# Kernel tuning notes

Hardware: AMD Instinct MI355X
Metric: run time of the kernel (lower is better)

## Reference

```python
import jax, jax.numpy as jnp
import numpy as np
from jax import lax


def ternarize(w):
    # TWN-style ternarization: threshold delta = 0.7*mean|w|, scale alpha =
    # mean |w| over surviving entries; straight-through in backward.
    aw = jnp.abs(w)
    delta = 0.7 * jnp.mean(aw)
    mask = (aw > delta).astype(w.dtype)
    alpha = jnp.sum(aw * mask) / jnp.maximum(jnp.sum(mask), 1.0)
    q = alpha * jnp.sign(w) * mask
    return w + lax.stop_gradient(q - w)


def conv2d(x, w, b):
    # x: [N,C,H,W], w: [O,I,kh,kw]
    y = lax.conv_general_dilated(x, w, window_strides=(1, 1), padding='VALID',
                                 dimension_numbers=('NCHW', 'OIHW', 'NCHW'))
    return y + b[None, :, None, None]


def maxpool2(x):
    return lax.reduce_window(x, -jnp.inf, lax.max,
                             window_dimensions=(1, 1, 2, 2),
                             window_strides=(1, 1, 2, 2), padding='VALID')


def setup_inputs() -> dict:
    key = jax.random.key(0)
    ks = jax.random.split(key, 11)
    n_classes = 10
    x = jax.random.normal(ks[0], (1024, 1, 32, 32), dtype=jnp.float32)
    # Kaiming-ish scaled params
    w1 = jax.random.normal(ks[1], (32, 1, 5, 5), jnp.float32) * (1.0 / np.sqrt(1 * 25))
    b1 = jnp.zeros((32,), jnp.float32)
    w2 = jax.random.normal(ks[2], (64, 32, 5, 5), jnp.float32) * (1.0 / np.sqrt(32 * 25))
    b2 = jnp.zeros((64,), jnp.float32)
    w3 = jax.random.normal(ks[3], (120, 64, 5, 5), jnp.float32) * (1.0 / np.sqrt(64 * 25))
    b3 = jnp.zeros((120,), jnp.float32)
    fw1 = jax.random.normal(ks[4], (84, 120), jnp.float32) * (1.0 / np.sqrt(120))
    fb1 = jnp.zeros((84,), jnp.float32)
    fw2 = jax.random.normal(ks[5], (n_classes, 84), jnp.float32) * (1.0 / np.sqrt(84))
    fb2 = jnp.zeros((n_classes,), jnp.float32)
    return {"x": x, "w1": w1, "b1": b1, "w2": w2, "b2": b2,
            "w3": w3, "b3": b3, "fw1": fw1, "fb1": fb1, "fw2": fw2, "fb2": fb2}


def reference(x, w1, b1, w2, b2, w3, b3, fw1, fb1, fw2, fb2):
    h = jnp.tanh(conv2d(x, ternarize(w1), b1))   # [N,32,28,28]
    h = maxpool2(h)                              # [N,32,14,14]
    h = jnp.tanh(conv2d(h, ternarize(w2), b2))   # [N,64,10,10]
    h = maxpool2(h)                              # [N,64,5,5]
    h = jnp.tanh(conv2d(h, ternarize(w3), b3))   # [N,120,1,1]
    h = h.reshape(h.shape[0], -1)                # [N,120]
    h = jnp.tanh(h @ ternarize(fw1).T + fb1)     # [N,84]
    logits = h @ ternarize(fw2).T + fb2          # [N,n_classes]
    probs = jax.nn.softmax(logits, axis=1)
    return (logits, probs)
```

## Files before the change

kernel.cpp:

```cpp
#include <hip/hip_runtime.h>
#include <hip/hip_bf16.h>
#include <math.h>


typedef __attribute__((ext_vector_type(8))) short bf16x8;
typedef __attribute__((ext_vector_type(4))) float f32x4;

static const size_t OFF_PB    = 0;
static const size_t OFF_W1B   = 256;
static const size_t OFF_W2B   = 1056;
static const size_t OFF_W3B   = 26656;
static const size_t OFF_FW1T  = 129056;
static const size_t OFF_FW2T  = 139136;
static const size_t OFF_P2B   = 139976;
static const size_t OFF_H3    = 959176;

#define BPT 16

__device__ __forceinline__ ushort f2bf(float v) {
    unsigned u = __float_as_uint(v);
    unsigned r = (u + 0x7FFFu + ((u >> 16) & 1u)) >> 16;
    return (ushort)r;
}
__device__ __forceinline__ float bf2f(ushort h) {
    return __uint_as_float((unsigned)h << 16);
}

__device__ __forceinline__ float tanh_fast(float x) {
    float e = __expf(-2.0f * fabsf(x));
    float r = 1.0f - 2.0f * e / (1.0f + e);
    return copysignf(r, x);
}

__device__ __forceinline__ void tensor_select(int tensor,
        const float* w1, const float* w2, const float* w3,
        const float* fw1, const float* fw2,
        const float*& src, int& O, int& K) {
    switch (tensor) {
        case 0: src = w1;  O = 32;  K = 25;   break;
        case 1: src = w2;  O = 64;  K = 800;  break;
        case 2: src = w3;  O = 120; K = 1600; break;
        case 3: src = fw1; O = 84;  K = 120;  break;
        default: src = fw2; O = 10; K = 84;   break;
    }
}

__device__ __forceinline__ float block_sum_256(float v, float* sbuf) {
    #pragma unroll
    for (int off = 32; off > 0; off >>= 1) v += __shfl_down(v, off);
    const int wid = threadIdx.x >> 6;
    if ((threadIdx.x & 63) == 0) sbuf[wid] = v;
    __syncthreads();
    return sbuf[0] + sbuf[1] + sbuf[2] + sbuf[3];
}

__device__ __forceinline__ float alpha_of(const float* pb, int tensor) {
    float s1 = 0.f, c = 0.f;
    #pragma unroll
    for (int i = 0; i < BPT; ++i) {
        s1 += pb[80 + tensor * BPT + i];
        c  += pb[160 + tensor * BPT + i];
    }
    return s1 / fmaxf(c, 1.0f);
}

__global__ __launch_bounds__(256)
void tern_pass1(const float* w1, const float* w2, const float* w3,
                const float* fw1, const float* fw2, float* pb) {
    __shared__ float sbuf[4];
    const int tensor = blockIdx.x / BPT;
    const int blk    = blockIdx.x % BPT;
    const float* src; int O, K;
    tensor_select(tensor, w1, w2, w3, fw1, fw2, src, O, K);
    const int n = O * K;
    float s = 0.f;
    for (int i = blk * 256 + threadIdx.x; i < n; i += BPT * 256)
        s += fabsf(src[i]);
    s = block_sum_256(s, sbuf);
    if (threadIdx.x == 0) pb[tensor * BPT + blk] = s;
}

__global__ __launch_bounds__(256)
void tern_pass2(const float* w1, const float* w2, const float* w3,
                const float* fw1, const float* fw2,
                ushort* w1b, ushort* w2b, ushort* w3b,
                float* fw1t, float* fw2t, float* pb) {
    __shared__ float sbuf[4];
    const int tensor = blockIdx.x / BPT;
    const int blk    = blockIdx.x % BPT;
    const float* src; int O, K;
    tensor_select(tensor, w1, w2, w3, fw1, fw2, src, O, K);
    const int n = O * K;
    float tot = 0.f;
    #pragma unroll
    for (int i = 0; i < BPT; ++i) tot += pb[tensor * BPT + i];
    const float delta = 0.7f * tot / (float)n;

    const ushort BP = 0x3F80u, BN = 0xBF80u;
    float s1 = 0.f, cnt = 0.f;

    if (tensor == 0) {
        for (int j = blk * 256 + threadIdx.x; j < 1024; j += BPT * 256) {
            const int oc = j >> 5, kk = j & 31;
            ushort qb = 0;
            if (kk < 25) {
                float w = src[oc * 25 + kk];
                float aw = fabsf(w);
                if (aw > delta) { s1 += aw; cnt += 1.f; qb = (w > 0.f) ? BP : BN; }
            }
            w1b[j] = qb;
        }
    } else if (tensor == 2) {
        for (int i = blk * 256 + threadIdx.x; i < 128 * 1600; i += BPT * 256) {
            ushort qb = 0;
            if (i < n) {
                float w = src[i];
                float aw = fabsf(w);
                if (aw > delta) { s1 += aw; cnt += 1.f; qb = (w > 0.f) ? BP : BN; }
            }
            w3b[i] = qb;
        }
    } else if (tensor == 1) {
        for (int i = blk * 256 + threadIdx.x; i < n; i += BPT * 256) {
            float w = src[i];
            float aw = fabsf(w);
            ushort qb = 0;
            if (aw > delta) { s1 += aw; cnt += 1.f; qb = (w > 0.f) ? BP : BN; }
            int oc = i / 800;
            int r  = i - oc * 800;
            int ic = r / 25;
            int tap = r - ic * 25;
            w2b[oc * 800 + tap * 32 + ic] = qb;
        }
    } else {
        float* dst = (tensor == 3) ? fw1t : fw2t;
        for (int i = blk * 256 + threadIdx.x; i < n; i += BPT * 256) {
            float w = src[i];
            float aw = fabsf(w);
            float q = 0.f;
            if (aw > delta) { s1 += aw; cnt += 1.f; q = (w > 0.f) ? 1.f : -1.f; }
            int o = i / K;
            int k = i - o * K;
            dst[k * O + o] = q;
        }
    }
    s1 = block_sum_256(s1, sbuf);
    __syncthreads();
    cnt = block_sum_256(cnt, sbuf);
    if (threadIdx.x == 0) {
        pb[80 + tensor * BPT + blk]  = s1;
        pb[160 + tensor * BPT + blk] = cnt;
    }
}

#define C2PF 4
__device__ __forceinline__ void conv2_all(
        const ushort* __restrict__ w2b, const ushort* sxt,
        int n0, int mt0, int lane, f32x4 acc[4][2]) {
    const int col = lane & 15, quad = lane >> 4;
    const ushort* abase[4];
    #pragma unroll
    for (int mi = 0; mi < 4; ++mi) {
        int m = (mt0 + mi) * 16 + col;
        m = m < 100 ? m : 99;
        const int oh = m / 10, ow = m - oh * 10;
        abase[mi] = sxt + (oh * 14 + ow) * 40 + quad * 8;
    }
    const ushort* wb0 = w2b + (size_t)(n0 + col) * 800 + quad * 8;
    const ushort* wb1 = wb0 + 16 * 800;
    bf16x8 pb0[C2PF], pb1[C2PF];
    #pragma unroll
    for (int i = 0; i < C2PF; ++i) {
        pb0[i] = *(const bf16x8*)(wb0 + i * 32);
        pb1[i] = *(const bf16x8*)(wb1 + i * 32);
    }
    #pragma unroll
    for (int tap = 0; tap < 25; ++tap) {
        const int slot = tap & (C2PF - 1);
        const bf16x8 b0 = pb0[slot];
        const bf16x8 b1 = pb1[slot];
        if (tap + C2PF < 25) {
            pb0[slot] = *(const bf16x8*)(wb0 + (tap + C2PF) * 32);
            pb1[slot] = *(const bf16x8*)(wb1 + (tap + C2PF) * 32);
        }
        const int kh = tap / 5, kw = tap - kh * 5;
        const int aoff = (kh * 14 + kw) * 40;
        #pragma unroll
        for (int mi = 0; mi < 4; ++mi) {
            bf16x8 af = *(const bf16x8*)(abase[mi] + aoff);
            acc[mi][0] = __builtin_amdgcn_mfma_f32_16x16x32_bf16(af, b0, acc[mi][0], 0, 0, 0);
            acc[mi][1] = __builtin_amdgcn_mfma_f32_16x16x32_bf16(af, b1, acc[mi][1], 0, 0, 0);
        }
    }
}

__global__ __launch_bounds__(256, 4)
void conv12_kernel(const float* __restrict__ x, const ushort* __restrict__ w1b,
                   const float* __restrict__ b1, const ushort* __restrict__ w2b,
                   const float* __restrict__ b2, const float* __restrict__ pb,
                   ushort* __restrict__ p2b) {
    __shared__ __align__(16) char smem[37328];
    ushort* A      = (ushort*)smem;
    float*  hb2    = (float*) smem;
    ushort* sxt    = (ushort*)(smem + 19584);
    ushort* sxb    = (ushort*)(smem + 35264);
    float*  salpha = (float*) (smem + 37312);

    const int n = blockIdx.x;
    const int t = threadIdx.x;
    const int wave = t >> 6, lane = t & 63;
    const int col = lane & 15, quad = lane >> 4;

    bf16x8 B0 = *(const bf16x8*)(w1b + col * 32 + quad * 8);
    bf16x8 B1 = *(const bf16x8*)(w1b + (col + 16) * 32 + quad * 8);
    const float b1a = b1[col];
    const float b1b = b1[col + 16];

    {
        float4 v = ((const float4*)(x + (size_t)n * 1024))[t];
        ushort4 q;
        q.x = f2bf(v.x); q.y = f2bf(v.y); q.z = f2bf(v.z); q.w = f2bf(v.w);
        *(ushort4*)(sxb + t * 4) = q;
        if (t == 0) salpha[0] = alpha_of(pb, 0);
        if (t == 1) salpha[1] = alpha_of(pb, 1);
    }
    __syncthreads();

    const float a1 = salpha[0];
    for (int c = 0; c < 3; ++c) {
        const int tbase = (c == 0) ? 0 : (17 + 16 * (c - 1));
        const int ct    = (c == 0) ? 17 : 16;
        const int pbase = tbase * 16;
        const int rows  = ct * 16;

        for (int r = t; r < rows; r += 256) {
            const int p   = pbase + r;
            const int pb4 = p >> 2, sub = p & 3;
            const int oh = 2 * (pb4 / 14) + (sub >> 1);
            const int ow = 2 * (pb4 % 14) + (sub & 1);
            ushort v[25];
            #pragma unroll
            for (int kh = 0; kh < 5; ++kh) {
                const ushort* rr = sxb + (oh + kh) * 32 + ow;
                v[kh*5+0]=rr[0]; v[kh*5+1]=rr[1]; v[kh*5+2]=rr[2];
                v[kh*5+3]=rr[3]; v[kh*5+4]=rr[4];
            }
            uint2* arow = (uint2*)(A + r * 36);
            #pragma unroll
            for (int j = 0; j < 6; ++j) {
                uint2 w;
                w.x = (unsigned)v[4*j]   | ((unsigned)v[4*j+1] << 16);
                w.y = (unsigned)v[4*j+2] | ((unsigned)v[4*j+3] << 16);
                arow[j] = w;
            }
            uint2 w6; w6.x = (unsigned)v[24]; w6.y = 0u;
            arow[6] = w6;
            uint2 w7; w7.x = 0u; w7.y = 0u;
            arow[7] = w7;
        }
        __syncthreads();

        for (int tl = wave; tl < ct; tl += 4) {
            const ushort* ap = A + (tl * 16 + col) * 36 + quad * 8;
            ushort4 lo = *(const ushort4*)ap;
            ushort4 hi = *(const ushort4*)(ap + 4);
            bf16x8 af;
            af[0]=(short)lo.x; af[1]=(short)lo.y; af[2]=(short)lo.z; af[3]=(short)lo.w;
            af[4]=(short)hi.x; af[5]=(short)hi.y; af[6]=(short)hi.z; af[7]=(short)hi.w;
            f32x4 z = {};
            f32x4 c0 = __builtin_amdgcn_mfma_f32_16x16x32_bf16(af, B0, z, 0, 0, 0);
            f32x4 c1 = __builtin_amdgcn_mfma_f32_16x16x32_bf16(af, B1, z, 0, 0, 0);
            const int pos2 = (pbase >> 2) + tl * 4 + quad;
            const float h01 = bf2f(f2bf(fmaxf(c0[0], c0[1])));
            const float h23 = bf2f(f2bf(fmaxf(c0[2], c0[3])));
            sxt[pos2 * 40 + col] =
                f2bf(tanh_fast(fmaf(a1, fmaxf(h01, h23), b1a)));
            const float g01 = bf2f(f2bf(fmaxf(c1[0], c1[1])));
            const float g23 = bf2f(f2bf(fmaxf(c1[2], c1[3])));
            sxt[pos2 * 40 + col + 16] =
                f2bf(tanh_fast(fmaf(a1, fmaxf(g01, g23), b1b)));
        }
        __syncthreads();
    }

    const int n0  = (wave & 1) * 32;
    const int mt0 = (wave >> 1) * 4;
    f32x4 acc2[4][2] = {};
    conv2_all(w2b, sxt, n0, mt0, lane, acc2);

    {
        #pragma unroll
        for (int mi = 0; mi < 4; ++mi) {
            const int mrow = (mt0 + mi) * 16 + quad * 4;
            if (mrow < 100) {
                #pragma unroll
                for (int np = 0; np < 2; ++np) {
                    const int oc = n0 + np * 16 + col;
                    float2 hm;
                    hm.x = fmaxf(acc2[mi][np][0], acc2[mi][np][1]);
                    hm.y = fmaxf(acc2[mi][np][2], acc2[mi][np][3]);
                    *(float2*)(&hb2[oc * 50 + (mrow >> 1)]) = hm;
                }
            }
        }
    }
    __syncthreads();

    const float a2 = salpha[1];
    for (int idx = t; idx < 1600; idx += 256) {
        const int oc = idx / 25, r = idx - oc * 25;
        const int ph = r / 5, pw = r - ph * 5;
        const float* hb = &hb2[oc * 50 + ph * 10 + pw];
        float m = fmaxf(hb[0], hb[5]);
        p2b[(size_t)n * 1600 + idx] = f2bf(tanh_fast(fmaf(a2, m, b2[oc])));
    }
}

template<int STEPS>
__device__ __forceinline__ void conv3_chunk(const ushort* Abase, const ushort* B0,
                                            f32x4& acc0) {
    #pragma unroll
    for (int s = 0; s < STEPS; ++s) {
        bf16x8 af = *(const bf16x8*)(Abase + s * 32);
        bf16x8 b0 = *(const bf16x8*)(B0 + s * 32);
        acc0 = __builtin_amdgcn_mfma_f32_16x16x32_bf16(af, b0, acc0, 0, 0, 0);
    }
}

__global__ __launch_bounds__(256)
void conv3_mfma(const ushort* __restrict__ p2b, const ushort* __restrict__ w3b,
                const float* __restrict__ b3, const float* __restrict__ pb,
                float* __restrict__ h3) {
    __shared__ float red[4][64][4];
    __shared__ float salpha;
    const int t = threadIdx.x;
    const int wave = t >> 6, lane = t & 63;
    const int mt   = blockIdx.x >> 3;
    const int noct = blockIdx.x & 7;
    const int col = lane & 15, quad = lane >> 4;
    const int kstart = (wave < 2) ? wave * 13 : 26 + (wave - 2) * 12;

    if (t == 0) salpha = alpha_of(pb, 2);

    const ushort* Abase = p2b + (size_t)(mt * 16 + col) * 1600 + kstart * 32 + quad * 8;
    const ushort* B0 = w3b + (size_t)(noct * 16 + col) * 1600 + kstart * 32 + quad * 8;

    f32x4 acc0 = {};
    if (wave < 2) conv3_chunk<13>(Abase, B0, acc0);
    else          conv3_chunk<12>(Abase, B0, acc0);

    #pragma unroll
    for (int r = 0; r < 4; ++r) red[wave][lane][r] = acc0[r];
    __syncthreads();

    {
        const float a3 = salpha;
        const int l = t & 63, vh = t >> 6;
        const int lcol = l & 15, lquad = l >> 4;
        const int img = mt * 16 + lquad * 4 + vh;
        float s = red[0][l][vh] + red[1][l][vh] + red[2][l][vh] + red[3][l][vh];
        const int oc = noct * 16 + lcol;
        if (oc < 120) h3[(size_t)img * 120 + oc] = tanh_fast(fmaf(a3, s, b3[oc]));
    }
}

__global__ __launch_bounds__(128)
void fc_kernel(const float* __restrict__ h3, const float* __restrict__ fw1t,
               const float* __restrict__ fb1, const float* __restrict__ fw2t,
               const float* __restrict__ fb2, const float* __restrict__ pb,
               float* __restrict__ out) {
    const int n = blockIdx.x;
    __shared__ float sh[120];
    __shared__ float sh4[84];
    __shared__ float sl[10];
    __shared__ float salpha[2];
    __shared__ __align__(16) float wbuf[2][30 * 84];
    __shared__ __align__(16) float fw2s[84 * 10];
    const int t = threadIdx.x;
    if (t < 120) sh[t] = h3[(size_t)n * 120 + t];
    if (t == 120) salpha[0] = alpha_of(pb, 3);
    if (t == 121) salpha[1] = alpha_of(pb, 4);
    #pragma unroll
    for (int i = 0; i < 2; ++i) {
        const int j = t + i * 128;
        if (j < 210) ((float4*)fw2s)[j] = ((const float4*)fw2t)[j];
    }
    for (int i = t; i < 630; i += 128)
        ((float4*)wbuf[0])[i] = ((const float4*)fw1t)[i];
    __syncthreads();

    float a = 0.f;
    #pragma unroll
    for (int c = 0; c < 4; ++c) {
        if (c < 3) {
            const float4* src = (const float4*)(fw1t + (c + 1) * 2520);
            float4* dst = (float4*)wbuf[(c + 1) & 1];
            for (int i = t; i < 630; i += 128) dst[i] = src[i];
        }
        if (t < 84) {
            const float* wc = wbuf[c & 1];
            #pragma unroll 6
            for (int kk = 0; kk < 30; ++kk)
                a = fmaf(wc[kk * 84 + t], sh[30 * c + kk], a);
        }
        __syncthreads();
    }
    if (t < 84) sh4[t] = tanh_fast(fmaf(salpha[0], a, fb1[t]));
    __syncthreads();
    if (t < 10) {
        const float af2 = salpha[1];
        float a2 = 0.f;
        #pragma unroll 4
        for (int k = 0; k < 84; ++k) a2 = fmaf(fw2s[k * 10 + t], sh4[k], a2);
        const float lg = fmaf(af2, a2, fb2[t]);
        sl[t] = lg;
        out[(size_t)n * 10 + t] = lg;
    }
    __syncthreads();
    if (t < 10) {
        float m = -INFINITY;
        #pragma unroll
        for (int i = 0; i < 10; ++i) m = fmaxf(m, sl[i]);
        float s = 0.f;
        #pragma unroll
        for (int i = 0; i < 10; ++i) s += expf(sl[i] - m);
        out[10240 + (size_t)n * 10 + t] = expf(sl[t] - m) / s;
    }
}

extern "C" void kernel_launch(void* const* d_in, const int* in_sizes, int n_in,
                              void* d_out, int out_size, void* d_ws, size_t ws_size,
                              hipStream_t stream) {
    const float* x   = (const float*)d_in[0];
    const float* w1  = (const float*)d_in[1];
    const float* b1  = (const float*)d_in[2];
    const float* w2  = (const float*)d_in[3];
    const float* b2  = (const float*)d_in[4];
    const float* w3  = (const float*)d_in[5];
    const float* b3  = (const float*)d_in[6];
    const float* fw1 = (const float*)d_in[7];
    const float* fb1 = (const float*)d_in[8];
    const float* fw2 = (const float*)d_in[9];
    const float* fb2 = (const float*)d_in[10];

    float* ws = (float*)d_ws;
    float*  pb   = ws + OFF_PB;
    ushort* w1b  = (ushort*)(ws + OFF_W1B);
    ushort* w2b  = (ushort*)(ws + OFF_W2B);
    ushort* w3b  = (ushort*)(ws + OFF_W3B);
    float*  fw1t = ws + OFF_FW1T;
    float*  fw2t = ws + OFF_FW2T;
    ushort* p2b  = (ushort*)(ws + OFF_P2B);
    float*  h3   = ws + OFF_H3;
    float*  out  = (float*)d_out;

    tern_pass1<<<5 * BPT, 256, 0, stream>>>(w1, w2, w3, fw1, fw2, pb);
    tern_pass2<<<5 * BPT, 256, 0, stream>>>(w1, w2, w3, fw1, fw2,
                                            w1b, w2b, w3b, fw1t, fw2t, pb);
    conv12_kernel<<<1024, 256, 0, stream>>>(x, w1b, b1, w2b, b2, pb, p2b);
    conv3_mfma<<<512, 256, 0, stream>>>(p2b, w3b, b3, pb, h3);
    fc_kernel<<<1024, 128, 0, stream>>>(h3, fw1t, fb1, fw2t, fb2, pb, out);
}
```

Baseline: 148.9 us.

## Fuse conv3 with FC layers and softmax into one kernel per 16 images

Merges the conv3 MFMA kernel and the per-image FC/softmax kernel into one kernel. Each block handles 16 images and all 8 output-channel tiles, keeps h3 in shared memory, and runs both FC layers and the softmax for those 16 images. This removes the h3 round trip through global memory and one launch, and it loads the FC weights once per 16 images instead of once per image. In exchange the grid shrinks from 512 and 1024 blocks to 64 blocks, which leaves most CUs idle, and the scalar FC loops are serialized within each block.

```diff
diff --git a/kernel.cpp b/kernel.cpp
--- a/kernel.cpp
+++ b/kernel.cpp
@@ -13,7 +13,6 @@
 static const size_t OFF_FW1T  = 129056;
 static const size_t OFF_FW2T  = 139136;
 static const size_t OFF_P2B   = 139976;
-static const size_t OFF_H3    = 959176;
 
 #define BPT 16
 
@@ -316,115 +315,105 @@
     }
 }
 
-template<int STEPS>
-__device__ __forceinline__ void conv3_chunk(const ushort* Abase, const ushort* B0,
-                                            f32x4& acc0) {
-    #pragma unroll
-    for (int s = 0; s < STEPS; ++s) {
-        bf16x8 af = *(const bf16x8*)(Abase + s * 32);
-        bf16x8 b0 = *(const bf16x8*)(B0 + s * 32);
-        acc0 = __builtin_amdgcn_mfma_f32_16x16x32_bf16(af, b0, acc0, 0, 0, 0);
-    }
-}
-
 __global__ __launch_bounds__(256)
-void conv3_mfma(const ushort* __restrict__ p2b, const ushort* __restrict__ w3b,
-                const float* __restrict__ b3, const float* __restrict__ pb,
-                float* __restrict__ h3) {
-    __shared__ float red[4][64][4];
-    __shared__ float salpha;
+void conv3fc_kernel(const ushort* __restrict__ p2b, const ushort* __restrict__ w3b,
+                    const float* __restrict__ b3, const float* __restrict__ pb,
+                    const float* __restrict__ fw1t, const float* __restrict__ fb1,
+                    const float* __restrict__ fw2t, const float* __restrict__ fb2,
+                    float* __restrict__ out) {
+    __shared__ __align__(16) char redmem[32768];
+    __shared__ __align__(16) float h3s[16][120];
+    __shared__ __align__(16) float fw1s[120 * 84];
+    __shared__ __align__(16) float fw2s[84 * 10];
+    __shared__ float salpha[3];
+    float (*red)[64][8][4] = (float (*)[64][8][4])redmem;
+    float* sh4 = (float*)redmem;
+    float* sl  = (float*)(redmem + 16 * 84 * 4);
+
     const int t = threadIdx.x;
     const int wave = t >> 6, lane = t & 63;
-    const int mt   = blockIdx.x >> 3;
-    const int noct = blockIdx.x & 7;
     const int col = lane & 15, quad = lane >> 4;
+    const int img0 = blockIdx.x * 16;
+
+    for (int i = t; i < 2520; i += 256)
+        ((float4*)fw1s)[i] = ((const float4*)fw1t)[i];
+    if (t < 210) ((float4*)fw2s)[t] = ((const float4*)fw2t)[t];
+    if (t == 0) salpha[0] = alpha_of(pb, 2);
+    if (t == 1) salpha[1] = alpha_of(pb, 3);
+    if (t == 2) salpha[2] = alpha_of(pb, 4);
+
     const int kstart = (wave < 2) ? wave * 13 : 26 + (wave - 2) * 12;
-
-    if (t == 0) salpha = alpha_of(pb, 2);
-
-    const ushort* Abase = p2b + (size_t)(mt * 16 + col) * 1600 + kstart * 32 + quad * 8;
-    const ushort* B0 = w3b + (size_t)(noct * 16 + col) * 1600 + kstart * 32 + quad * 8;
-
-    f32x4 acc0 = {};
-    if (wave < 2) conv3_chunk<13>(Abase, B0, acc0);
-    else          conv3_chunk<12>(Abase, B0, acc0);
-
-    #pragma unroll
-    for (int r = 0; r < 4; ++r) red[wave][lane][r] = acc0[r];
+    const int steps  = (wave < 2) ? 13 : 12;
+    const ushort* Abase = p2b + (size_t)(img0 + col) * 1600 + kstart * 32 + quad * 8;
+    const ushort* Bbase = w3b + (size_t)col * 1600 + kstart * 32 + quad * 8;
+
+    f32x4 acc[8] = {};
+    for (int s = 0; s < steps; ++s) {
+        const bf16x8 af = *(const bf16x8*)(Abase + s * 32);
+        #pragma unroll
+        for (int nt = 0; nt < 8; ++nt) {
+            const bf16x8 bf = *(const bf16x8*)(Bbase + (size_t)nt * 16 * 1600 + s * 32);
+            acc[nt] = __builtin_amdgcn_mfma_f32_16x16x32_bf16(af, bf, acc[nt], 0, 0, 0);
+        }
+    }
+    #pragma unroll
+    for (int nt = 0; nt < 8; ++nt)
+        #pragma unroll
+        for (int r = 0; r < 4; ++r) red[wave][lane][nt][r] = acc[nt][r];
     __syncthreads();
 
     {
-        const float a3 = salpha;
+        const float a3 = salpha[0];
         const int l = t & 63, vh = t >> 6;
         const int lcol = l & 15, lquad = l >> 4;
-        const int img = mt * 16 + lquad * 4 + vh;
-        float s = red[0][l][vh] + red[1][l][vh] + red[2][l][vh] + red[3][l][vh];
-        const int oc = noct * 16 + lcol;
-        if (oc < 120) h3[(size_t)img * 120 + oc] = tanh_fast(fmaf(a3, s, b3[oc]));
-    }
-}
-
-__global__ __launch_bounds__(128)
-void fc_kernel(const float* __restrict__ h3, const float* __restrict__ fw1t,
-               const float* __restrict__ fb1, const float* __restrict__ fw2t,
-               const float* __restrict__ fb2, const float* __restrict__ pb,
-               float* __restrict__ out) {
-    const int n = blockIdx.x;
-    __shared__ float sh[120];
-    __shared__ float sh4[84];
-    __shared__ float sl[10];
-    __shared__ float salpha[2];
-    __shared__ __align__(16) float wbuf[2][30 * 84];
-    __shared__ __align__(16) float fw2s[84 * 10];
-    const int t = threadIdx.x;
-    if (t < 120) sh[t] = h3[(size_t)n * 120 + t];
-    if (t == 120) salpha[0] = alpha_of(pb, 3);
-    if (t == 121) salpha[1] = alpha_of(pb, 4);
-    #pragma unroll
-    for (int i = 0; i < 2; ++i) {
-        const int j = t + i * 128;
-        if (j < 210) ((float4*)fw2s)[j] = ((const float4*)fw2t)[j];
-    }
-    for (int i = t; i < 630; i += 128)
-        ((float4*)wbuf[0])[i] = ((const float4*)fw1t)[i];
-    __syncthreads();
-
-    float a = 0.f;
-    #pragma unroll
-    for (int c = 0; c < 4; ++c) {
-        if (c < 3) {
-            const float4* src = (const float4*)(fw1t + (c + 1) * 2520);
-            float4* dst = (float4*)wbuf[(c + 1) & 1];
-            for (int i = t; i < 630; i += 128) dst[i] = src[i];
-        }
-        if (t < 84) {
-            const float* wc = wbuf[c & 1];
-            #pragma unroll 6
-            for (int kk = 0; kk < 30; ++kk)
-                a = fmaf(wc[kk * 84 + t], sh[30 * c + kk], a);
-        }
-        __syncthreads();
-    }
-    if (t < 84) sh4[t] = tanh_fast(fmaf(salpha[0], a, fb1[t]));
-    __syncthreads();
-    if (t < 10) {
-        const float af2 = salpha[1];
+        const int img = lquad * 4 + vh;
+        #pragma unroll
+        for (int nt = 0; nt < 8; ++nt) {
+            const int oc = nt * 16 + lcol;
+            if (oc < 120) {
+                float s = red[0][l][nt][vh] + red[1][l][nt][vh]
+                        + red[2][l][nt][vh] + red[3][l][nt][vh];
+                h3s[img][oc] = tanh_fast(fmaf(a3, s, b3[oc]));
+            }
+        }
+    }
+    __syncthreads();
+
+    {
+        const float af1 = salpha[1];
+        for (int task = t; task < 1344; task += 256) {
+            const int img = task / 84, oc = task - img * 84;
+            float a = 0.f;
+            #pragma unroll 4
+            for (int k = 0; k < 120; ++k)
+                a = fmaf(fw1s[k * 84 + oc], h3s[img][k], a);
+            sh4[img * 84 + oc] = tanh_fast(fmaf(af1, a, fb1[oc]));
+        }
+    }
+    __syncthreads();
+
+    if (t < 160) {
+        const float af2 = salpha[2];
+        const int img = t / 10, oc = t - img * 10;
         float a2 = 0.f;
         #pragma unroll 4
-        for (int k = 0; k < 84; ++k) a2 = fmaf(fw2s[k * 10 + t], sh4[k], a2);
-        const float lg = fmaf(af2, a2, fb2[t]);
-        sl[t] = lg;
-        out[(size_t)n * 10 + t] = lg;
-    }
-    __syncthreads();
-    if (t < 10) {
+        for (int k = 0; k < 84; ++k)
+            a2 = fmaf(fw2s[k * 10 + oc], sh4[img * 84 + k], a2);
+        const float lg = fmaf(af2, a2, fb2[oc]);
+        sl[img * 10 + oc] = lg;
+        out[(size_t)(img0 + img) * 10 + oc] = lg;
+    }
+    __syncthreads();
+
+    if (t < 160) {
+        const int img = t / 10, oc = t - img * 10;
         float m = -INFINITY;
         #pragma unroll
-        for (int i = 0; i < 10; ++i) m = fmaxf(m, sl[i]);
+        for (int i = 0; i < 10; ++i) m = fmaxf(m, sl[img * 10 + i]);
         float s = 0.f;
         #pragma unroll
-        for (int i = 0; i < 10; ++i) s += expf(sl[i] - m);
-        out[10240 + (size_t)n * 10 + t] = expf(sl[t] - m) / s;
+        for (int i = 0; i < 10; ++i) s += expf(sl[img * 10 + i] - m);
+        out[10240 + (size_t)(img0 + img) * 10 + oc] = expf(sl[img * 10 + oc] - m) / s;
     }
 }
 
@@ -451,13 +440,12 @@
     float*  fw1t = ws + OFF_FW1T;
     float*  fw2t = ws + OFF_FW2T;
     ushort* p2b  = (ushort*)(ws + OFF_P2B);
-    float*  h3   = ws + OFF_H3;
     float*  out  = (float*)d_out;
 
     tern_pass1<<<5 * BPT, 256, 0, stream>>>(w1, w2, w3, fw1, fw2, pb);
     tern_pass2<<<5 * BPT, 256, 0, stream>>>(w1, w2, w3, fw1, fw2,
                                             w1b, w2b, w3b, fw1t, fw2t, pb);
     conv12_kernel<<<1024, 256, 0, stream>>>(x, w1b, b1, w2b, b2, pb, p2b);
-    conv3_mfma<<<512, 256, 0, stream>>>(p2b, w3b, b3, pb, h3);
-    fc_kernel<<<1024, 128, 0, stream>>>(h3, fw1t, fb1, fw2t, fb2, pb, out);
-}
+    conv3fc_kernel<<<64, 256, 0, stream>>>(p2b, w3b, b3, pb,
+                                           fw1t, fb1, fw2t, fb2, out);
+}
```

New measurement: 160.3 us. 7.7% more time.
